# Optimization experiments

Hardware: AMD Instinct MI355X
Metric: run time of the kernel (lower is better)

## Reference

```python
import jax, jax.numpy as jnp
import numpy as np

U, I = 200000, 100000
E = 9600000
D = 64
T_LAYERS = 3   # transformer_layers
N_LAYERS = 3   # n_layers


def setup_inputs() -> dict:
    key = jax.random.key(0)
    k1, k2, k3, k4, k5 = jax.random.split(key, 5)
    user_emb = jax.random.normal(k1, (U, D), dtype=jnp.float32) * (2.0 / (U + D)) ** 0.5
    item_emb = jax.random.normal(k2, (I, D), dtype=jnp.float32) * (2.0 / (I + D)) ** 0.5
    N = U + I
    row = jax.random.randint(k3, (E,), 0, N, dtype=jnp.int32)
    col = jax.random.randint(k4, (E,), 0, N, dtype=jnp.int32)
    # positive normalized-adjacency-like values
    vals = jax.random.uniform(k5, (E,), dtype=jnp.float32) * 0.01
    return {"user_emb": user_emb, "item_emb": item_emb, "row": row, "col": col, "vals": vals}


def _spmm(row, col, vals, x, n):
    # sparse [n,n] @ dense [n,d] via gather + segment_sum
    return jax.ops.segment_sum(vals[:, None] * x[col], row, num_segments=n)


def reference(user_emb, item_emb, row, col, vals):
    n = user_emb.shape[0] + item_emb.shape[0]
    e0 = jnp.concatenate([user_emb, item_emb], axis=0)  # [N, D]
    embs = [e0]
    hs = [e0]
    h = e0
    for layer in range(T_LAYERS):
        h = _spmm(row, col, vals, h, n)
        hs.append(h)
        if layer < N_LAYERS:
            embs.append(h)
    # main mean over [e0, h1, ..., h_min(T,L)]
    mean_all = jnp.mean(jnp.stack(embs, axis=1), axis=1)
    users, items = mean_all[:U], mean_all[U:]
    # embs_mean[i] = [e0, h1, ..., h_{i+1}] -> cumulative running mean
    users_mean, items_mean = [], []
    csum = hs[0]
    for i in range(T_LAYERS):
        csum = csum + hs[i + 1]
        m = csum / float(i + 2)
        users_mean.append(m[:U])
        items_mean.append(m[U:])
    return (users, items, *users_mean, *items_mean)
```

## Files before the change

### kernel.cpp

```cpp
#include <hip/hip_runtime.h>
#include <hip/hip_fp16.h>

constexpr int U = 200000;
constexpr int I = 100000;
constexpr int N = 300000;
constexpr int E = 9600000;
constexpr int D4 = 16;
constexpr int D8 = 8;

constexpr int NBKT  = 32;
constexpr int RSPAN = N / NBKT;
constexpr int CAP1  = 310000;
constexpr int FPC   = 64;
constexpr int NF    = NBKT * FPC;
constexpr int FR    = 147;
constexpr int FCAP  = 5504;
constexpr int NSUB  = 40;

constexpr int NCB   = 32;
constexpr int CSPAN = (N + NCB - 1) / NCB;
constexpr int NKEY  = FR * NCB;

constexpr int K4_E0 = 9;
constexpr int K4_H1 = 14;
constexpr int K4_H2 = 19;

constexpr float VQ_ENC = 819100.0f;
constexpr float VQ_DEC = 0.01f / 8191.0f;

typedef float f32x4 __attribute__((ext_vector_type(4)));
typedef float f32x2 __attribute__((ext_vector_type(2)));

#if __has_builtin(__builtin_amdgcn_cvt_pk_f32_fp8)
#define FP8_HW 1
constexpr int FP8_EXTRA = 0;
#else
constexpr int FP8_EXTRA = 120;
#endif

__device__ __forceinline__ float pow2f(int x) {
    return __uint_as_float((unsigned)(127 + x) << 23);
}

__device__ __forceinline__ void nt_store4(float4 v, float4* p) {
    f32x4 w = {v.x, v.y, v.z, v.w};
    __builtin_nontemporal_store(w, (f32x4*)p);
}

__device__ __forceinline__ unsigned short f2bf(float f) {
    unsigned int u = __float_as_uint(f);
    unsigned int r = (u + 0x7fffu + ((u >> 16) & 1u)) >> 16;
    return (unsigned short)r;
}
__device__ __forceinline__ unsigned int packbf(float lo, float hi) {
    return (unsigned int)f2bf(lo) | ((unsigned int)f2bf(hi) << 16);
}
__device__ __forceinline__ float bflo(unsigned int w) { return __uint_as_float(w << 16); }
__device__ __forceinline__ float bfhi(unsigned int w) { return __uint_as_float(w & 0xffff0000u); }

__device__ __forceinline__ unsigned f2fp4(float y) {
    unsigned s = (__float_as_uint(y) >> 28) & 0x8u;
    float a = fabsf(y);
    unsigned q = (unsigned)(a >= 0.25f) + (a >= 0.75f) + (a >= 1.25f) + (a >= 1.75f)
               + (a >= 2.5f) + (a >= 3.5f) + (a >= 5.0f);
    return s | q;
}
__device__ __forceinline__ unsigned pack8f4(const float a[8], float sc) {
    return f2fp4(a[0] * sc)        | (f2fp4(a[4] * sc) << 4)  |
           (f2fp4(a[1] * sc) << 8) | (f2fp4(a[5] * sc) << 12) |
           (f2fp4(a[2] * sc) << 16)| (f2fp4(a[6] * sc) << 20) |
           (f2fp4(a[3] * sc) << 24)| (f2fp4(a[7] * sc) << 28);
}

__device__ __forceinline__ unsigned nib2f8(unsigned x) {
#if __has_builtin(__builtin_amdgcn_perm)
    unsigned mag = __builtin_amdgcn_perm(0x4C484440u, 0x3C383000u, x & 0x07070707u);
    return mag | ((x & 0x08080808u) << 4);
#else
    unsigned r = 0;
#pragma unroll
    for (int k = 0; k < 4; ++k) {
        unsigned n = (x >> (8 * k)) & 0xFu;
        unsigned m = n & 7u, e = m >> 1;
        unsigned mag = e ? (((e + 6u) << 3) | ((m & 1u) << 2)) : ((m & 1u) ? 0x30u : 0u);
        r |= (mag | ((n & 8u) << 4)) << (8 * k);
    }
    return r;
#endif
}

__device__ __forceinline__ void acc8f4(float a[8], unsigned w, float vs) {
    unsigned f8lo = nib2f8(w & 0x0F0F0F0Fu);
    unsigned f8hi = nib2f8((w >> 4) & 0x0F0F0F0Fu);
#ifdef FP8_HW
    f32x2 p;
    p = __builtin_amdgcn_cvt_pk_f32_fp8((int)f8lo, false);
    a[0] = fmaf(vs, p.x, a[0]); a[1] = fmaf(vs, p.y, a[1]);
    p = __builtin_amdgcn_cvt_pk_f32_fp8((int)f8lo, true);
    a[2] = fmaf(vs, p.x, a[2]); a[3] = fmaf(vs, p.y, a[3]);
    p = __builtin_amdgcn_cvt_pk_f32_fp8((int)f8hi, false);
    a[4] = fmaf(vs, p.x, a[4]); a[5] = fmaf(vs, p.y, a[5]);
    p = __builtin_amdgcn_cvt_pk_f32_fp8((int)f8hi, true);
    a[6] = fmaf(vs, p.x, a[6]); a[7] = fmaf(vs, p.y, a[7]);
#else
    unsigned ws[2] = {f8lo, f8hi};
#pragma unroll
    for (int h = 0; h < 2; ++h) {
#pragma unroll
        for (int j = 0; j < 4; ++j) {
            unsigned b = (ws[h] >> (8 * j)) & 0xffu;
            float r = __uint_as_float(((b & 0x80u) << 24) | ((b & 0x7fu) << 20));
            a[h * 4 + j] = fmaf(vs, r, a[h * 4 + j]);
        }
    }
#endif
}


__global__ void init_cursors(int* __restrict__ bktCur, int* __restrict__ fineCur) {
    int t = blockIdx.x * blockDim.x + threadIdx.x;
    if (t < NBKT) bktCur[t] = t * CAP1;
    if (t < NF) fineCur[t] = t * FCAP;
}

__global__ void bucket1(const int* __restrict__ row, const int* __restrict__ col,
                        const float* __restrict__ vals, int* __restrict__ bktCur,
                        int2* __restrict__ cA) {
    __shared__ int cnt[NBKT];
    __shared__ int fill[NBKT];
    __shared__ int lofs[NBKT + 1];
    __shared__ int goff[NBKT];
    __shared__ int2 st[1024];
    __shared__ unsigned char bktS[1024];

    int tid = threadIdx.x;
    int base = blockIdx.x * 1024;
    if (tid < NBKT) { cnt[tid] = 0; fill[tid] = 0; }
    __syncthreads();

    int r[4], c[4], b[4];
    float v[4];
#pragma unroll
    for (int i = 0; i < 4; ++i) {
        int e = base + tid + i * 256;
        r[i] = row[e];
        c[i] = col[e];
        v[i] = vals[e];
        b[i] = r[i] / RSPAN;
        atomicAdd(&cnt[b[i]], 1);
    }
    __syncthreads();
    if (tid == 0) {
        int s = 0;
        for (int k = 0; k < NBKT; ++k) { lofs[k] = s; s += cnt[k]; }
        lofs[NBKT] = s;
    }
    __syncthreads();
    if (tid < NBKT) goff[tid] = atomicAdd(&bktCur[tid], cnt[tid]);
    __syncthreads();
#pragma unroll
    for (int i = 0; i < 4; ++i) {
        int p = lofs[b[i]] + atomicAdd(&fill[b[i]], 1);
        unsigned q = (unsigned)rintf(v[i] * VQ_ENC);
        unsigned w0 = (unsigned)r[i] | (((unsigned)c[i] & 0x1FFFu) << 19);
        unsigned w1 = ((unsigned)c[i] >> 13) | (q << 6);
        st[p] = make_int2((int)w0, (int)w1);
        bktS[p] = (unsigned char)b[i];
    }
    __syncthreads();
    for (int i = tid; i < 1024; i += 256) {
        int bb = bktS[i];
        cA[goff[bb] + (i - lofs[bb])] = st[i];
    }
}

__global__ void bucket2(const int2* __restrict__ cA, const int* __restrict__ bktCur,
                        int* __restrict__ fineCur, int2* __restrict__ fA) {
    __shared__ int cnt[FPC];
    __shared__ int fill[FPC];
    __shared__ int lofs[FPC + 1];
    __shared__ int goff[FPC];
    __shared__ int2 st[1024];
    __shared__ unsigned char fbS[1024];

    int cb = blockIdx.x & (NBKT - 1);
    int sub = blockIdx.x >> 5;
    int tid = threadIdx.x;
    int s0 = cb * CAP1;
    int end = bktCur[cb];

    for (int base = s0 + sub * 1024; base < end; base += NSUB * 1024) {
        int m = min(1024, end - base);
        if (tid < FPC) { cnt[tid] = 0; fill[tid] = 0; }
        __syncthreads();

        int2 e[4];
        int fb[4];
#pragma unroll
        for (int i = 0; i < 4; ++i) {
            int j = tid + i * 256;
            if (j < m) {
                e[i] = cA[base + j];
                int rr = (int)((unsigned)e[i].x & 0x7FFFFu);
                fb[i] = (rr - cb * RSPAN) / FR;
                atomicAdd(&cnt[fb[i]], 1);
            } else {
                fb[i] = -1;
            }
        }
        __syncthreads();
        if (tid == 0) {
            int s = 0;
            for (int k = 0; k < FPC; ++k) { lofs[k] = s; s += cnt[k]; }
            lofs[FPC] = s;
        }
        __syncthreads();
        if (tid < FPC) goff[tid] = atomicAdd(&fineCur[cb * FPC + tid], cnt[tid]);
        __syncthreads();
#pragma unroll
        for (int i = 0; i < 4; ++i) {
            if (fb[i] >= 0) {
                unsigned w0 = (unsigned)e[i].x, w1 = (unsigned)e[i].y;
                int rr = (int)(w0 & 0x7FFFFu);
                unsigned c = (w0 >> 19) | ((w1 & 0x3Fu) << 13);
                unsigned q = (w1 >> 6) & 0x1FFFu;
                int rloc = rr - cb * RSPAN - fb[i] * FR;
                int p = lofs[fb[i]] + atomicAdd(&fill[fb[i]], 1);
                st[p] = make_int2((int)(c | (q << 19)), rloc);
                fbS[p] = (unsigned char)fb[i];
            }
        }
        __syncthreads();
        int total = lofs[FPC];
        for (int i = tid; i < total; i += 256) {
            int bb = fbS[i];
            fA[goff[bb] + (i - lofs[bb])] = st[i];
        }
        __syncthreads();
    }
}

__global__ void fine_scan(const int* __restrict__ fineCur, int* __restrict__ fineBase) {
    __shared__ int ts[256];
    int tid = threadIdx.x;
    int vals[8];
    int sum = 0;
#pragma unroll
    for (int k = 0; k < 8; ++k) {
        int f = tid * 8 + k;
        vals[k] = sum;
        sum += fineCur[f] - f * FCAP;
    }
    ts[tid] = sum;
    __syncthreads();
    for (int off = 1; off < 256; off <<= 1) {
        int t = (tid >= off) ? ts[tid - off] : 0;
        __syncthreads();
        ts[tid] += t;
        __syncthreads();
    }
    int excl = tid ? ts[tid - 1] : 0;
#pragma unroll
    for (int k = 0; k < 8; ++k) fineBase[tid * 8 + k] = excl + vals[k];
}

__global__ __launch_bounds__(1024) void scatter3(const int2* __restrict__ fA,
                                                 const int* __restrict__ fineCur,
                                                 const int* __restrict__ fineBase,
                                                 unsigned* __restrict__ edgeS,
                                                 int* __restrict__ rowPtr) {
    __shared__ int lcnt[NKEY];
    __shared__ int ts[1024];
    int fbk = blockIdx.x;
    int tid = threadIdx.x;
    for (int i = tid; i < NKEY; i += 1024) lcnt[i] = 0;
    __syncthreads();
    int s = fbk * FCAP;
    int m = fineCur[fbk] - s;
    for (int i = tid; i < m; i += 1024) {
        int2 ev = fA[s + i];
        int cb = (int)((unsigned)ev.x & 0x7FFFFu) / CSPAN;
        atomicAdd(&lcnt[ev.y * NCB + cb], 1);
    }
    __syncthreads();
    constexpr int PER = (NKEY + 1023) / 1024;
    int loc[PER];
    int sum = 0;
#pragma unroll
    for (int k = 0; k < PER; ++k) {
        int idx = tid * PER + k;
        int v = (idx < NKEY) ? lcnt[idx] : 0;
        loc[k] = sum;
        sum += v;
    }
    ts[tid] = sum;
    __syncthreads();
    for (int off2 = 1; off2 < 1024; off2 <<= 1) {
        int t2 = (tid >= off2) ? ts[tid - off2] : 0;
        __syncthreads();
        ts[tid] += t2;
        __syncthreads();
    }
    int excl = tid ? ts[tid - 1] : 0;
#pragma unroll
    for (int k = 0; k < PER; ++k) {
        int idx = tid * PER + k;
        if (idx < NKEY) lcnt[idx] = excl + loc[k];
    }
    __syncthreads();
    int base = fineBase[fbk];
    int cb_ = fbk >> 6, fb_ = fbk & 63;
    int rbase = cb_ * RSPAN + fb_ * FR;
    int rows = min(FR, RSPAN - fb_ * FR);
    for (int r = tid; r < rows; r += 1024) rowPtr[rbase + r] = base + lcnt[r * NCB];
    if (fbk == NF - 1 && tid == 0) rowPtr[N] = base + m;
    __syncthreads();
    for (int i = tid; i < m; i += 1024) {
        int2 ev = fA[s + i];
        int cb2 = (int)((unsigned)ev.x & 0x7FFFFu) / CSPAN;
        int pos = base + atomicAdd(&lcnt[ev.y * NCB + cb2], 1);
        edgeS[pos] = (unsigned)ev.x;
    }
}

__global__ void conv_e0(const float4* __restrict__ ue, const float4* __restrict__ ie,
                        unsigned* __restrict__ e0f4, uint4* __restrict__ e0bf) {
    size_t j = (size_t)blockIdx.x * blockDim.x + threadIdx.x;
    constexpr size_t N8 = (size_t)N * D8;
    constexpr size_t U16 = (size_t)U * D4;
    if (j >= N8) return;
    size_t f4 = j * 2;
    float4 f0, f1;
    if (f4 < U16) { f0 = ue[f4]; f1 = ue[f4 + 1]; }
    else          { f0 = ie[f4 - U16]; f1 = ie[f4 + 1 - U16]; }
    float a[8] = {f0.x, f0.y, f0.z, f0.w, f1.x, f1.y, f1.z, f1.w};
    e0f4[j] = pack8f4(a, pow2f(K4_E0));
    uint4 ob;
    ob.x = packbf(a[0], a[1]); ob.y = packbf(a[2], a[3]);
    ob.z = packbf(a[4], a[5]); ob.w = packbf(a[6], a[7]);
    e0bf[j] = ob;
}


__global__ void spmm_f4(const int* __restrict__ rowPtr, const unsigned* __restrict__ edgeS,
                        const unsigned* __restrict__ xf4, const uint4* __restrict__ sInBf,
                        uint4* __restrict__ sOutBf, unsigned* __restrict__ yf4,
                        int kIn, int kOut) {
    int lane = threadIdx.x & 7;
    int n = blockIdx.x * 32 + (threadIdx.x >> 3);
    int s = rowPtr[n], t = rowPtr[n + 1];
    const float invS2 = pow2f(FP8_EXTRA - kIn) * VQ_DEC;
    float a[8] = {0.f, 0.f, 0.f, 0.f, 0.f, 0.f, 0.f, 0.f};
    int e = s;
    if (t - s >= 8) {
        unsigned ev[8];
#pragma unroll
        for (int k = 0; k < 8; ++k) ev[k] = edgeS[e + k];
        e += 8;
        while (e + 8 <= t) {
            unsigned x[8];
#pragma unroll
            for (int k = 0; k < 8; ++k) x[k] = xf4[(size_t)(ev[k] & 0x7FFFFu) * D8 + lane];
            unsigned nx[8];
#pragma unroll
            for (int k = 0; k < 8; ++k) nx[k] = edgeS[e + k];
#pragma unroll
            for (int k = 0; k < 8; ++k) acc8f4(a, x[k], (float)(ev[k] >> 19) * invS2);
#pragma unroll
            for (int k = 0; k < 8; ++k) ev[k] = nx[k];
            e += 8;
        }
        unsigned x[8];
#pragma unroll
        for (int k = 0; k < 8; ++k) x[k] = xf4[(size_t)(ev[k] & 0x7FFFFu) * D8 + lane];
#pragma unroll
        for (int k = 0; k < 8; ++k) acc8f4(a, x[k], (float)(ev[k] >> 19) * invS2);
    }
    for (; e < t; ++e) {
        unsigned ev = edgeS[e];
        unsigned x = xf4[(size_t)(ev & 0x7FFFFu) * D8 + lane];
        acc8f4(a, x, (float)(ev >> 19) * invS2);
    }
    size_t r8 = (size_t)n * D8 + lane;
    uint4 si = sInBf[r8];
    float sv[8];
    sv[0] = bflo(si.x) + a[0]; sv[1] = bfhi(si.x) + a[1];
    sv[2] = bflo(si.y) + a[2]; sv[3] = bfhi(si.y) + a[3];
    sv[4] = bflo(si.z) + a[4]; sv[5] = bfhi(si.z) + a[5];
    sv[6] = bflo(si.w) + a[6]; sv[7] = bfhi(si.w) + a[7];
    uint4 so;
    so.x = packbf(sv[0], sv[1]); so.y = packbf(sv[2], sv[3]);
    so.z = packbf(sv[4], sv[5]); so.w = packbf(sv[6], sv[7]);
    sOutBf[r8] = so;
    yf4[r8] = pack8f4(a, pow2f(kOut));
}

__global__ void spmm_final(const int* __restrict__ rowPtr, const unsigned* __restrict__ edgeS,
                           const unsigned* __restrict__ h2f4, const uint4* __restrict__ s1bf,
                           const uint4* __restrict__ s2bf, float4* __restrict__ out) {
    int lane = threadIdx.x & 7;
    int n = blockIdx.x * 32 + (threadIdx.x >> 3);
    int s = rowPtr[n], t = rowPtr[n + 1];
    const float invS2 = pow2f(FP8_EXTRA - K4_H2) * VQ_DEC;
    float a[8] = {0.f, 0.f, 0.f, 0.f, 0.f, 0.f, 0.f, 0.f};
    int e = s;
    if (t - s >= 8) {
        unsigned ev[8];
#pragma unroll
        for (int k = 0; k < 8; ++k) ev[k] = edgeS[e + k];
        e += 8;
        while (e + 8 <= t) {
            unsigned x[8];
#pragma unroll
            for (int k = 0; k < 8; ++k) x[k] = h2f4[(size_t)(ev[k] & 0x7FFFFu) * D8 + lane];
            unsigned nx[8];
#pragma unroll
            for (int k = 0; k < 8; ++k) nx[k] = edgeS[e + k];
#pragma unroll
            for (int k = 0; k < 8; ++k) acc8f4(a, x[k], (float)(ev[k] >> 19) * invS2);
#pragma unroll
            for (int k = 0; k < 8; ++k) ev[k] = nx[k];
            e += 8;
        }
        unsigned x[8];
#pragma unroll
        for (int k = 0; k < 8; ++k) x[k] = h2f4[(size_t)(ev[k] & 0x7FFFFu) * D8 + lane];
#pragma unroll
        for (int k = 0; k < 8; ++k) acc8f4(a, x[k], (float)(ev[k] >> 19) * invS2);
    }
    for (; e < t; ++e) {
        unsigned ev = edgeS[e];
        unsigned x = h2f4[(size_t)(ev & 0x7FFFFu) * D8 + lane];
        acc8f4(a, x, (float)(ev >> 19) * invS2);
    }

    size_t r8 = (size_t)n * D8 + lane;
    uint4 w1 = s1bf[r8];
    uint4 w2 = s2bf[r8];
    float s1v[8], s2v[8];
    s1v[0] = bflo(w1.x); s1v[1] = bfhi(w1.x); s1v[2] = bflo(w1.y); s1v[3] = bfhi(w1.y);
    s1v[4] = bflo(w1.z); s1v[5] = bfhi(w1.z); s1v[6] = bflo(w1.w); s1v[7] = bfhi(w1.w);
    s2v[0] = bflo(w2.x); s2v[1] = bfhi(w2.x); s2v[2] = bflo(w2.y); s2v[3] = bfhi(w2.y);
    s2v[4] = bflo(w2.z); s2v[5] = bfhi(w2.z); s2v[6] = bflo(w2.w); s2v[7] = bfhi(w2.w);

    float4 um0a, um0b, um1a, um1b, ma, mb;
    um0a.x = s1v[0] * 0.5f;  um0a.y = s1v[1] * 0.5f;  um0a.z = s1v[2] * 0.5f;  um0a.w = s1v[3] * 0.5f;
    um0b.x = s1v[4] * 0.5f;  um0b.y = s1v[5] * 0.5f;  um0b.z = s1v[6] * 0.5f;  um0b.w = s1v[7] * 0.5f;
    um1a.x = s2v[0] / 3.0f;  um1a.y = s2v[1] / 3.0f;  um1a.z = s2v[2] / 3.0f;  um1a.w = s2v[3] / 3.0f;
    um1b.x = s2v[4] / 3.0f;  um1b.y = s2v[5] / 3.0f;  um1b.z = s2v[6] / 3.0f;  um1b.w = s2v[7] / 3.0f;
    ma.x = (s2v[0] + a[0]) * 0.25f; ma.y = (s2v[1] + a[1]) * 0.25f;
    ma.z = (s2v[2] + a[2]) * 0.25f; ma.w = (s2v[3] + a[3]) * 0.25f;
    mb.x = (s2v[4] + a[4]) * 0.25f; mb.y = (s2v[5] + a[5]) * 0.25f;
    mb.z = (s2v[6] + a[6]) * 0.25f; mb.w = (s2v[7] + a[7]) * 0.25f;

    constexpr size_t N16 = (size_t)N * D4;
    constexpr size_t U16 = (size_t)U * D4;
    constexpr size_t I16 = (size_t)I * D4;
    if (n < U) {
        size_t r = (size_t)n * D4 + lane * 2;
        nt_store4(ma,   &out[r]);
        nt_store4(mb,   &out[r + 1]);
        nt_store4(um0a, &out[N16 + r]);
        nt_store4(um0b, &out[N16 + r + 1]);
        nt_store4(um1a, &out[N16 + U16 + r]);
        nt_store4(um1b, &out[N16 + U16 + r + 1]);
        nt_store4(ma,   &out[N16 + 2 * U16 + r]);
        nt_store4(mb,   &out[N16 + 2 * U16 + r + 1]);
    } else {
        size_t r = (size_t)(n - U) * D4 + lane * 2;
        nt_store4(ma,   &out[U16 + r]);
        nt_store4(mb,   &out[U16 + r + 1]);
        nt_store4(um0a, &out[N16 + 3 * U16 + r]);
        nt_store4(um0b, &out[N16 + 3 * U16 + r + 1]);
        nt_store4(um1a, &out[N16 + 3 * U16 + I16 + r]);
        nt_store4(um1b, &out[N16 + 3 * U16 + I16 + r + 1]);
        nt_store4(ma,   &out[N16 + 3 * U16 + 2 * I16 + r]);
        nt_store4(mb,   &out[N16 + 3 * U16 + 2 * I16 + r + 1]);
    }
}

extern "C" void kernel_launch(void* const* d_in, const int* in_sizes, int n_in,
                              void* d_out, int out_size, void* d_ws, size_t ws_size,
                              hipStream_t stream) {
    const float* ue   = (const float*)d_in[0];
    const float* ie   = (const float*)d_in[1];
    const int*   row  = (const int*)d_in[2];
    const int*   col  = (const int*)d_in[3];
    const float* vals = (const float*)d_in[4];

    char* ws = (char*)d_ws;
    size_t off = 0;
    char* regA = ws + off; off += (size_t)3 * E * 4;
    char* regB = ws + off; off += (size_t)NBKT * CAP1 * 8;
    char* regC = ws + off; off += (size_t)N * 64 * 2;
    int* rowPtr   = (int*)(ws + off); off += (size_t)(N + 1) * 4;
    int* bktCur   = (int*)(ws + off); off += 128;
    int* fineCur  = (int*)(ws + off); off += (size_t)NF * 4;
    int* fineBase = (int*)(ws + off); off += (size_t)NF * 4;

    constexpr size_t F4B = (size_t)N * 32;
    int2*     fA    = (int2*)regA;
    unsigned* e0f4  = (unsigned*)regA;
    unsigned* h1f4  = (unsigned*)(regA + F4B);
    unsigned* h2f4  = (unsigned*)(regA + 2 * F4B);
    uint4*    s1bf  = (uint4*)(regA + 3 * F4B);
    uint4*    s2bf  = (uint4*)regC;
    int2*     cA    = (int2*)regB;
    unsigned* edgeS = (unsigned*)regB;
    uint4*    e0bf  = (uint4*)(regB + (size_t)E * 4);

    init_cursors<<<(NF + 255) / 256, 256, 0, stream>>>(bktCur, fineCur);
    bucket1<<<E / 1024, 256, 0, stream>>>(row, col, vals, bktCur, cA);
    bucket2<<<NBKT * NSUB, 256, 0, stream>>>(cA, bktCur, fineCur, fA);
    fine_scan<<<1, 256, 0, stream>>>(fineCur, fineBase);
    scatter3<<<NF, 1024, 0, stream>>>(fA, fineCur, fineBase, edgeS, rowPtr);

    const size_t n8 = (size_t)N * D8;
    conv_e0<<<(int)((n8 + 255) / 256), 256, 0, stream>>>((const float4*)ue, (const float4*)ie,
                                                         e0f4, e0bf);

    const int spmmBlocks = N / 32;
    spmm_f4<<<spmmBlocks, 256, 0, stream>>>(rowPtr, edgeS, e0f4, e0bf, s1bf, h1f4,
                                            K4_E0, K4_H1);
    spmm_f4<<<spmmBlocks, 256, 0, stream>>>(rowPtr, edgeS, h1f4, s1bf, s2bf, h2f4,
                                            K4_H1, K4_H2);
    spmm_final<<<spmmBlocks, 256, 0, stream>>>(rowPtr, edgeS, h2f4, s1bf, s2bf,
                                               (float4*)d_out);
}
```

Measured before the change: 714.4 us.

## Split SpMM feature dimension into four planes to shrink gather working set

Stores the FP4 and bf16 embedding arrays in four feature-plane layouts (16 features per plane) and runs each SpMM as four passes, one per plane, with 2 threads per row instead of 8. Each pass gathers from a quarter-sized table, so the random column gathers are meant to fit better in the L2/MALL cache. The cost is re-reading rowPtr and edge indices four times per layer and launching more kernels. Scatter3 also keeps the edge words and keys in LDS so the second pass does not reread global memory.

```diff
diff --git a/kernel.cpp b/kernel.cpp
--- a/kernel.cpp
+++ b/kernel.cpp
@@ -27,6 +27,9 @@
 
 constexpr float VQ_ENC = 819100.0f;
 constexpr float VQ_DEC = 0.01f / 8191.0f;
+
+constexpr size_t PL4 = (size_t)N * 2;
+constexpr size_t PLB = (size_t)N * 2;
 
 typedef float f32x4 __attribute__((ext_vector_type(4)));
 typedef float f32x2 __attribute__((ext_vector_type(2)));
@@ -271,6 +274,8 @@
                                                  int* __restrict__ rowPtr) {
     __shared__ int lcnt[NKEY];
     __shared__ int ts[1024];
+    __shared__ unsigned stW[FCAP];
+    __shared__ unsigned short stK[FCAP];
     int fbk = blockIdx.x;
     int tid = threadIdx.x;
     for (int i = tid; i < NKEY; i += 1024) lcnt[i] = 0;
@@ -279,8 +284,11 @@
     int m = fineCur[fbk] - s;
     for (int i = tid; i < m; i += 1024) {
         int2 ev = fA[s + i];
-        int cb = (int)((unsigned)ev.x & 0x7FFFFu) / CSPAN;
-        atomicAdd(&lcnt[ev.y * NCB + cb], 1);
+        unsigned w = (unsigned)ev.x;
+        int key = ev.y * NCB + (int)(w & 0x7FFFFu) / CSPAN;
+        stW[i] = w;
+        stK[i] = (unsigned short)key;
+        atomicAdd(&lcnt[key], 1);
     }
     __syncthreads();
     constexpr int PER = (NKEY + 1023) / 1024;
@@ -316,10 +324,9 @@
     if (fbk == NF - 1 && tid == 0) rowPtr[N] = base + m;
     __syncthreads();
     for (int i = tid; i < m; i += 1024) {
-        int2 ev = fA[s + i];
-        int cb2 = (int)((unsigned)ev.x & 0x7FFFFu) / CSPAN;
-        int pos = base + atomicAdd(&lcnt[ev.y * NCB + cb2], 1);
-        edgeS[pos] = (unsigned)ev.x;
+        int k = stK[i];
+        int pos = base + atomicAdd(&lcnt[k], 1);
+        edgeS[pos] = stW[i];
     }
 }
 
@@ -334,20 +341,24 @@
     if (f4 < U16) { f0 = ue[f4]; f1 = ue[f4 + 1]; }
     else          { f0 = ie[f4 - U16]; f1 = ie[f4 + 1 - U16]; }
     float a[8] = {f0.x, f0.y, f0.z, f0.w, f1.x, f1.y, f1.z, f1.w};
-    e0f4[j] = pack8f4(a, pow2f(K4_E0));
+    size_t n = j >> 3;
+    int g = (int)(j & 7);
+    size_t dst = (size_t)(g >> 1) * PL4 + n * 2 + (g & 1);
+    e0f4[dst] = pack8f4(a, pow2f(K4_E0));
     uint4 ob;
     ob.x = packbf(a[0], a[1]); ob.y = packbf(a[2], a[3]);
     ob.z = packbf(a[4], a[5]); ob.w = packbf(a[6], a[7]);
-    e0bf[j] = ob;
+    e0bf[(size_t)(g >> 1) * PLB + n * 2 + (g & 1)] = ob;
 }
 
 
 __global__ void spmm_f4(const int* __restrict__ rowPtr, const unsigned* __restrict__ edgeS,
-                        const unsigned* __restrict__ xf4, const uint4* __restrict__ sInBf,
-                        uint4* __restrict__ sOutBf, unsigned* __restrict__ yf4,
+                        const unsigned* __restrict__ xf4p, const uint4* __restrict__ sInP,
+                        uint4* __restrict__ sOutP, unsigned* __restrict__ yf4p,
                         int kIn, int kOut) {
-    int lane = threadIdx.x & 7;
-    int n = blockIdx.x * 32 + (threadIdx.x >> 3);
+    int l = threadIdx.x & 1;
+    int n = blockIdx.x * 128 + (threadIdx.x >> 1);
+    if (n >= N) return;
     int s = rowPtr[n], t = rowPtr[n + 1];
     const float invS2 = pow2f(FP8_EXTRA - kIn) * VQ_DEC;
     float a[8] = {0.f, 0.f, 0.f, 0.f, 0.f, 0.f, 0.f, 0.f};
@@ -360,7 +371,7 @@
         while (e + 8 <= t) {
             unsigned x[8];
 #pragma unroll
-            for (int k = 0; k < 8; ++k) x[k] = xf4[(size_t)(ev[k] & 0x7FFFFu) * D8 + lane];
+            for (int k = 0; k < 8; ++k) x[k] = xf4p[(size_t)(ev[k] & 0x7FFFFu) * 2 + l];
             unsigned nx[8];
 #pragma unroll
             for (int k = 0; k < 8; ++k) nx[k] = edgeS[e + k];
@@ -372,17 +383,17 @@
         }
         unsigned x[8];
 #pragma unroll
-        for (int k = 0; k < 8; ++k) x[k] = xf4[(size_t)(ev[k] & 0x7FFFFu) * D8 + lane];
+        for (int k = 0; k < 8; ++k) x[k] = xf4p[(size_t)(ev[k] & 0x7FFFFu) * 2 + l];
 #pragma unroll
         for (int k = 0; k < 8; ++k) acc8f4(a, x[k], (float)(ev[k] >> 19) * invS2);
     }
     for (; e < t; ++e) {
         unsigned ev = edgeS[e];
-        unsigned x = xf4[(size_t)(ev & 0x7FFFFu) * D8 + lane];
+        unsigned x = xf4p[(size_t)(ev & 0x7FFFFu) * 2 + l];
         acc8f4(a, x, (float)(ev >> 19) * invS2);
     }
-    size_t r8 = (size_t)n * D8 + lane;
-    uint4 si = sInBf[r8];
+    size_t r2 = (size_t)n * 2 + l;
+    uint4 si = sInP[r2];
     float sv[8];
     sv[0] = bflo(si.x) + a[0]; sv[1] = bfhi(si.x) + a[1];
     sv[2] = bflo(si.y) + a[2]; sv[3] = bfhi(si.y) + a[3];
@@ -391,15 +402,16 @@
     uint4 so;
     so.x = packbf(sv[0], sv[1]); so.y = packbf(sv[2], sv[3]);
     so.z = packbf(sv[4], sv[5]); so.w = packbf(sv[6], sv[7]);
-    sOutBf[r8] = so;
-    yf4[r8] = pack8f4(a, pow2f(kOut));
+    sOutP[r2] = so;
+    yf4p[r2] = pack8f4(a, pow2f(kOut));
 }
 
 __global__ void spmm_final(const int* __restrict__ rowPtr, const unsigned* __restrict__ edgeS,
-                           const unsigned* __restrict__ h2f4, const uint4* __restrict__ s1bf,
-                           const uint4* __restrict__ s2bf, float4* __restrict__ out) {
-    int lane = threadIdx.x & 7;
-    int n = blockIdx.x * 32 + (threadIdx.x >> 3);
+                           const unsigned* __restrict__ h2f4p, const uint4* __restrict__ s1P,
+                           const uint4* __restrict__ s2P, float4* __restrict__ out, int p) {
+    int l = threadIdx.x & 1;
+    int n = blockIdx.x * 128 + (threadIdx.x >> 1);
+    if (n >= N) return;
     int s = rowPtr[n], t = rowPtr[n + 1];
     const float invS2 = pow2f(FP8_EXTRA - K4_H2) * VQ_DEC;
     float a[8] = {0.f, 0.f, 0.f, 0.f, 0.f, 0.f, 0.f, 0.f};
@@ -412,7 +424,7 @@
         while (e + 8 <= t) {
             unsigned x[8];
 #pragma unroll
-            for (int k = 0; k < 8; ++k) x[k] = h2f4[(size_t)(ev[k] & 0x7FFFFu) * D8 + lane];
+            for (int k = 0; k < 8; ++k) x[k] = h2f4p[(size_t)(ev[k] & 0x7FFFFu) * 2 + l];
             unsigned nx[8];
 #pragma unroll
             for (int k = 0; k < 8; ++k) nx[k] = edgeS[e + k];
@@ -424,19 +436,19 @@
         }
         unsigned x[8];
 #pragma unroll
-        for (int k = 0; k < 8; ++k) x[k] = h2f4[(size_t)(ev[k] & 0x7FFFFu) * D8 + lane];
+        for (int k = 0; k < 8; ++k) x[k] = h2f4p[(size_t)(ev[k] & 0x7FFFFu) * 2 + l];
 #pragma unroll
         for (int k = 0; k < 8; ++k) acc8f4(a, x[k], (float)(ev[k] >> 19) * invS2);
     }
     for (; e < t; ++e) {
         unsigned ev = edgeS[e];
-        unsigned x = h2f4[(size_t)(ev & 0x7FFFFu) * D8 + lane];
+        unsigned x = h2f4p[(size_t)(ev & 0x7FFFFu) * 2 + l];
         acc8f4(a, x, (float)(ev >> 19) * invS2);
     }
 
-    size_t r8 = (size_t)n * D8 + lane;
-    uint4 w1 = s1bf[r8];
-    uint4 w2 = s2bf[r8];
+    size_t r2 = (size_t)n * 2 + l;
+    uint4 w1 = s1P[r2];
+    uint4 w2 = s2P[r2];
     float s1v[8], s2v[8];
     s1v[0] = bflo(w1.x); s1v[1] = bfhi(w1.x); s1v[2] = bflo(w1.y); s1v[3] = bfhi(w1.y);
     s1v[4] = bflo(w1.z); s1v[5] = bfhi(w1.z); s1v[6] = bflo(w1.w); s1v[7] = bfhi(w1.w);
@@ -456,8 +468,9 @@
     constexpr size_t N16 = (size_t)N * D4;
     constexpr size_t U16 = (size_t)U * D4;
     constexpr size_t I16 = (size_t)I * D4;
+    int q = 4 * p + 2 * l;
     if (n < U) {
-        size_t r = (size_t)n * D4 + lane * 2;
+        size_t r = (size_t)n * D4 + q;
         nt_store4(ma,   &out[r]);
         nt_store4(mb,   &out[r + 1]);
         nt_store4(um0a, &out[N16 + r]);
@@ -467,7 +480,7 @@
         nt_store4(ma,   &out[N16 + 2 * U16 + r]);
         nt_store4(mb,   &out[N16 + 2 * U16 + r + 1]);
     } else {
-        size_t r = (size_t)(n - U) * D4 + lane * 2;
+        size_t r = (size_t)(n - U) * D4 + q;
         nt_store4(ma,   &out[U16 + r]);
         nt_store4(mb,   &out[U16 + r + 1]);
         nt_store4(um0a, &out[N16 + 3 * U16 + r]);
@@ -519,11 +532,17 @@
     conv_e0<<<(int)((n8 + 255) / 256), 256, 0, stream>>>((const float4*)ue, (const float4*)ie,
                                                          e0f4, e0bf);
 
-    const int spmmBlocks = N / 32;
-    spmm_f4<<<spmmBlocks, 256, 0, stream>>>(rowPtr, edgeS, e0f4, e0bf, s1bf, h1f4,
-                                            K4_E0, K4_H1);
-    spmm_f4<<<spmmBlocks, 256, 0, stream>>>(rowPtr, edgeS, h1f4, s1bf, s2bf, h2f4,
-                                            K4_H1, K4_H2);
-    spmm_final<<<spmmBlocks, 256, 0, stream>>>(rowPtr, edgeS, h2f4, s1bf, s2bf,
-                                               (float4*)d_out);
-}
+    const int spmmBlocks = (N + 127) / 128;
+    for (int p = 0; p < 4; ++p)
+        spmm_f4<<<spmmBlocks, 256, 0, stream>>>(rowPtr, edgeS, e0f4 + p * PL4,
+                                                e0bf + p * PLB, s1bf + p * PLB,
+                                                h1f4 + p * PL4, K4_E0, K4_H1);
+    for (int p = 0; p < 4; ++p)
+        spmm_f4<<<spmmBlocks, 256, 0, stream>>>(rowPtr, edgeS, h1f4 + p * PL4,
+                                                s1bf + p * PLB, s2bf + p * PLB,
+                                                h2f4 + p * PL4, K4_H1, K4_H2);
+    for (int p = 0; p < 4; ++p)
+        spmm_final<<<spmmBlocks, 256, 0, stream>>>(rowPtr, edgeS, h2f4 + p * PL4,
+                                                   s1bf + p * PLB, s2bf + p * PLB,
+                                                   (float4*)d_out, p);
+}
```

Result: slower. 1.055 ms (+47.7%).
